# Optimization experiments

Measured on AMD Instinct MI355X. Metric: run time of the kernel, lower is better.

The kernel has to match this reference:

```python
import jax, jax.numpy as jnp
import numpy as np
from itertools import product

N = 300000          # active voxels
CIN, C = 16, 32     # input / conv channels
K = 27              # 3x3x3 kernel volume
Z, Y, X = 41, 1024, 1024  # sparse spatial shape (grid_size[::-1] + [1,0,0])
B = 2               # batch size
EPS = 1e-3          # BatchNorm eps (matches norm_fn eps=0.001)


def _build_coords_and_rulebook(rng):
    # unique active coords per batch element
    total = Z * Y * X
    per = N // B
    coords = []
    for b in range(B):
        lin = np.unique(rng.integers(0, total, size=int(per * 1.3)))
        rng.shuffle(lin)
        lin = lin[:per]
        assert lin.shape[0] == per
        z = lin // (Y * X)
        y = (lin % (Y * X)) // X
        x = lin % X
        coords.append(np.stack([np.full(per, b), z, y, x], axis=1))
    coords = np.concatenate(coords, axis=0).astype(np.int64)  # [N,4]

    # hash-free rulebook via sorted linear keys + searchsorted
    key = ((coords[:, 0] * Z + coords[:, 1]) * Y + coords[:, 2]) * X + coords[:, 3]
    perm = np.argsort(key)
    skey = key[perm]
    nbr = np.full((N, K), -1, dtype=np.int32)
    bz, zz, yy, xx = coords[:, 0], coords[:, 1], coords[:, 2], coords[:, 3]
    for k, (dz, dy, dx) in enumerate(product((-1, 0, 1), repeat=3)):
        nz, ny, nx = zz + dz, yy + dy, xx + dx
        valid = (nz >= 0) & (nz < Z) & (ny >= 0) & (ny < Y) & (nx >= 0) & (nx < X)
        nkey = ((bz * Z + nz) * Y + ny) * X + nx
        pos = np.searchsorted(skey, nkey)
        pos = np.clip(pos, 0, N - 1)
        found = valid & (skey[pos] == nkey)
        nbr[:, k] = np.where(found, perm[pos], -1).astype(np.int32)
    return coords, nbr


def _bn_params(k, c):
    k1, k2, k3, k4 = jax.random.split(k, 4)
    gamma = jax.random.uniform(k1, (c,), minval=0.5, maxval=1.5)
    beta = jax.random.normal(k2, (c,)) * 0.1
    mean = jax.random.normal(k3, (c,)) * 0.1
    var = jax.random.uniform(k4, (c,), minval=0.5, maxval=1.5)
    return jnp.stack([gamma, beta, mean, var], axis=0)  # [4,C]


def setup_inputs() -> dict:
    rng = np.random.default_rng(0)
    _, nbr = _build_coords_and_rulebook(rng)

    key = jax.random.key(0)
    ks = jax.random.split(key, 12)
    feat = jax.random.normal(ks[0], (N, CIN), dtype=jnp.float32)

    def conv_w(k, cin, cout):
        return jax.random.normal(k, (K, cin, cout), dtype=jnp.float32) * (1.0 / np.sqrt(K * cin))

    return {
        "voxel_features": feat,
        "neighbor_idx": jnp.asarray(nbr),
        "w_in": conv_w(ks[1], CIN, C), "bn_in": _bn_params(ks[2], C),
        "w1a": conv_w(ks[3], C, C), "bn1a": _bn_params(ks[4], C),
        "w1b": conv_w(ks[5], C, C), "bn1b": _bn_params(ks[6], C),
        "w2a": conv_w(ks[7], C, C), "bn2a": _bn_params(ks[8], C),
        "w2b": conv_w(ks[9], C, C), "bn2b": _bn_params(ks[10], C),
    }


def reference(voxel_features, neighbor_idx, w_in, bn_in, w1a, bn1a, w1b, bn1b,
              w2a, bn2a, w2b, bn2b):
    def bn(x, p):
        gamma, beta, mean, var = p
        return gamma * (x - mean) * jax.lax.rsqrt(var + EPS) + beta

    def subm(feat, w):
        # submanifold conv: gather active neighbors, GEMM per kernel offset, accumulate
        out = jnp.zeros((feat.shape[0], w.shape[2]), feat.dtype)
        for k in range(K):
            idx = neighbor_idx[:, k]
            g = jnp.where((idx >= 0)[:, None], feat[jnp.maximum(idx, 0)], 0.0)
            out = out + g @ w[k]
        return out

    # conv_input: SubMConv3d + BN + ReLU
    x = jax.nn.relu(bn(subm(voxel_features, w_in), bn_in))
    # conv1: two SparseBasicBlocks (conv-bn-relu-conv-bn + residual, relu)
    for wa, bna, wb, bnb in ((w1a, bn1a, w1b, bn1b), (w2a, bn2a, w2b, bn2b)):
        identity = x
        x = jax.nn.relu(bn(subm(x, wa), bna))
        x = bn(subm(x, wb), bnb)
        x = jax.nn.relu(x + identity)
    # voxel importance (vis_importance branch, minus file IO / sorting side effects)
    voxel_importance = jax.nn.sigmoid(jnp.mean(jnp.abs(x), axis=1, keepdims=True))
    return x, voxel_importance
```

## Files before the change

### kernel.cpp

```cpp
#include <hip/hip_runtime.h>
#include <hip/hip_bf16.h>
#include <hip/hip_fp16.h>
#include <cstdint>
#include <cstddef>

#define NVOX 300000
#define KNBR 27
#define COUT 32
#define CINP 32
#define NT   (NVOX / 16)
#define RB   ((NVOX + 255) / 256)
#define WFIXE (5 * KNBR * CINP * COUT)
#define WFB  ((WFIXE + 255) / 256)
#define WDE  (5 * COUT * CINP)
#define WDB  ((WDE + 255) / 256)
#define WPL  (KNBR * CINP * COUT)
#define GD   1172
#define GF0  876

typedef __hip_bfloat16 bf16;
typedef _Float16 half8 __attribute__((ext_vector_type(8)));
typedef float floatx4 __attribute__((ext_vector_type(4)));
typedef unsigned short ushort8 __attribute__((ext_vector_type(8)));

__device__ __forceinline__ float bf2f(unsigned short u) {
    union { unsigned int i; float f; } x; x.i = ((unsigned int)u) << 16; return x.f;
}
__device__ __forceinline__ int detect_fp32(const void* b0) {
    const unsigned short* p = (const unsigned short*)b0;
    int hits = 0;
    for (int i = 0; i < 16; i++) {
        float v = bf2f(p[2 * i]);
        if (v >= 0.25f && v <= 4.0f) hits++;
    }
    return (hits >= 8) ? 0 : 1;
}
__device__ __forceinline__ float rdw(const void* w, int rel, int fp32) {
    return fp32 ? ((const float*)w)[rel] : __bfloat162float(((const bf16*)w)[rel]);
}


__global__ __launch_bounds__(256)
void setup_kernel(const int* __restrict__ nbr,
                  const void* w0, const void* w1, const void* w2, const void* w3, const void* w4,
                  const void* b0, const void* b1, const void* b2, const void* b3, const void* b4,
                  float* __restrict__ wfix, __half* __restrict__ wtf,
                  float* __restrict__ bnab,
                  int* __restrict__ flag, int* __restrict__ counter,
                  int* __restrict__ cvlist, int* __restrict__ corrpos) {
    const int tid = threadIdx.x;

    if (blockIdx.x < RB) {
        __shared__ int flags[256];
        __shared__ int wsum[4];
        __shared__ int wbase[4];
        flags[tid] = 0;
        __syncthreads();
        const int base = blockIdx.x * 256;
        const int nvox = (NVOX - base < 256) ? (NVOX - base) : 256;
        const int nI4  = (nvox * KNBR) >> 2;
        const int4* p4 = (const int4*)(nbr + (size_t)base * KNBR);
        for (int i = tid; i < nI4; i += 256) {
            const int4 q = p4[i];
            if ((q.x & q.y & q.z & q.w) < 0) continue;
            const unsigned t = (unsigned)(i << 2);
            if (q.x >= 0) { unsigned u = t;     unsigned lv = (u * 4855u) >> 17; if (u - lv * 27u != 13u) flags[lv] = 1; }
            if (q.y >= 0) { unsigned u = t + 1; unsigned lv = (u * 4855u) >> 17; if (u - lv * 27u != 13u) flags[lv] = 1; }
            if (q.z >= 0) { unsigned u = t + 2; unsigned lv = (u * 4855u) >> 17; if (u - lv * 27u != 13u) flags[lv] = 1; }
            if (q.w >= 0) { unsigned u = t + 3; unsigned lv = (u * 4855u) >> 17; if (u - lv * 27u != 13u) flags[lv] = 1; }
        }
        __syncthreads();
        const int v = base + tid;
        const bool f = (tid < nvox) && (flags[tid] != 0);
        const unsigned long long wm = __ballot(f);
        const int wd = tid >> 6, ln = tid & 63;
        if (ln == 0) wsum[wd] = __popcll(wm);
        __syncthreads();
        if (tid == 0) {
            int t0 = wsum[0], t1 = wsum[1], t2 = wsum[2], t3 = wsum[3];
            int tot = t0 + t1 + t2 + t3;
            int b = tot ? atomicAdd(counter, tot) : 0;
            wbase[0] = b; wbase[1] = b + t0; wbase[2] = b + t0 + t1; wbase[3] = b + t0 + t1 + t2;
        }
        __syncthreads();
        if (f) {
            int pos = wbase[wd] + __popcll(wm & ((1ULL << ln) - 1ULL));
            cvlist[pos] = v;
            corrpos[v]  = pos;
        }
        return;
    }

    const int fp32 = detect_fp32(b0);

    if (blockIdx.x < RB + WFB) {
        int i = (blockIdx.x - RB) * 256 + tid;
        if (i >= WFIXE) return;
        int L   = i / (KNBR * CINP * COUT);
        int rem = i % (KNBR * CINP * COUT);
        int k   = rem / (CINP * COUT);
        int kk  = (rem / COUT) % CINP;
        int nn  = rem % COUT;
        const void* w = (L == 0) ? w0 : (L == 1) ? w1 : (L == 2) ? w2 : (L == 3) ? w3 : w4;
        int cinL = (L == 0) ? 16 : 32;
        wfix[i] = (kk < cinL) ? rdw(w, (k * cinL + kk) * COUT + nn, fp32) : 0.f;
        return;
    }

    if (blockIdx.x < RB + WFB + WDB) {
        int i = (blockIdx.x - RB - WFB) * 256 + tid;
        if (i >= WDE) return;
        int L  = i / (COUT * CINP);
        int nn = (i / CINP) % COUT;
        int kk = i % CINP;
        const void* w = (L == 0) ? w0 : (L == 1) ? w1 : (L == 2) ? w2 : (L == 3) ? w3 : w4;
        int cinL = (L == 0) ? 16 : 32;
        int sk = (L == 0) ? kk : ((kk & 1) ? 16 + (kk >> 1) : (kk >> 1));
        float val = (sk < cinL) ? rdw(w, (13 * cinL + sk) * COUT + nn, fp32) : 0.f;
        wtf[i] = __float2half(val);
        return;
    }

    if (tid == 192) *flag = fp32;
    if (tid < 160) {
        int L = tid / 32, c = tid % 32;
        const void* b = (L == 0) ? b0 : (L == 1) ? b1 : (L == 2) ? b2 : (L == 3) ? b3 : b4;
        float g, be, m, v;
        if (fp32) {
            const float* q = (const float*)b;
            g = q[c]; be = q[32 + c]; m = q[64 + c]; v = q[96 + c];
        } else {
            const bf16* q = (const bf16*)b;
            g = __bfloat162float(q[c]); be = __bfloat162float(q[32 + c]);
            m = __bfloat162float(q[64 + c]); v = __bfloat162float(q[96 + c]);
        }
        float a = g * rsqrtf(v + 1e-3f);
        bnab[L * 64 + c]      = a;
        bnab[L * 64 + 32 + c] = be - a * m;
    }
}


struct DW {
    half8 wa[5], wb[5];
    float ba[5], bb[5], bc[5], bd[5];
};
__device__ __forceinline__ void load_dw(DW& d, const __half* __restrict__ wtf,
                                        const float* __restrict__ bnab, int n, int quad) {
#pragma unroll
    for (int L = 0; L < 5; L++) {
        d.wa[L] = *(const half8*)((const _Float16*)wtf + L * 1024 + n * 32 + quad * 8);
        d.wb[L] = *(const half8*)((const _Float16*)wtf + L * 1024 + (n + 16) * 32 + quad * 8);
        d.ba[L] = bnab[L * 64 + n];      d.bb[L] = bnab[L * 64 + 32 + n];
        d.bc[L] = bnab[L * 64 + 16 + n]; d.bd[L] = bnab[L * 64 + 48 + n];
    }
}

__device__ __forceinline__ void dense_range(
    int gw, int nw, const DW& dw,
    const void* __restrict__ feat, int fp32, void* __restrict__ out_base,
    _Float16 (* __restrict__ myT)[40], int n, int quad) {
    for (int t = gw; t < NT; t += nw) {
        const int v0 = t * 16;
        half8 af = {};
        if (quad < 2) {
            if (fp32) {
                const float* p = (const float*)feat + (size_t)(v0 + n) * 16 + quad * 8;
                const float4 u0 = *(const float4*)p;
                const float4 u1 = *(const float4*)(p + 4);
                af[0] = (_Float16)u0.x; af[1] = (_Float16)u0.y; af[2] = (_Float16)u0.z; af[3] = (_Float16)u0.w;
                af[4] = (_Float16)u1.x; af[5] = (_Float16)u1.y; af[6] = (_Float16)u1.z; af[7] = (_Float16)u1.w;
            } else {
                const ushort8 u = *(const ushort8*)((const unsigned short*)feat + (size_t)(v0 + n) * 16 + quad * 8);
#pragma unroll
                for (int j = 0; j < 8; j++) af[j] = (_Float16)bf2f(u[j]);
            }
        }
        float id0[4], id1[4];
#pragma unroll
        for (int L = 0; L < 5; L++) {
            floatx4 c0 = {0.f, 0.f, 0.f, 0.f}, c1 = {0.f, 0.f, 0.f, 0.f};
            c0 = __builtin_amdgcn_mfma_f32_16x16x32_f16(af, dw.wa[L], c0, 0, 0, 0);
            c1 = __builtin_amdgcn_mfma_f32_16x16x32_f16(af, dw.wb[L], c1, 0, 0, 0);
            if (L < 4) {
#pragma unroll
                for (int r = 0; r < 4; r++) {
                    float y0 = fmaf(dw.ba[L], c0[r], dw.bb[L]);
                    float y1 = fmaf(dw.bc[L], c1[r], dw.bd[L]);
                    if (L == 2) { y0 += id0[r]; y1 += id1[r]; }
                    y0 = fmaxf(y0, 0.f); y1 = fmaxf(y1, 0.f);
                    if (L == 0 || L == 2) { id0[r] = y0; id1[r] = y1; }
                    const int m = quad * 4 + r;
                    *reinterpret_cast<__half2*>(&myT[m][2 * n]) = __floats2half2_rn(y0, y1);
                }
                af = *reinterpret_cast<const half8*>(&myT[n][quad * 8]);
            } else {
#pragma unroll
                for (int r = 0; r < 4; r++) {
                    float y0 = fmaxf(fmaf(dw.ba[4], c0[r], dw.bb[4]) + id0[r], 0.f);
                    float y1 = fmaxf(fmaf(dw.bc[4], c1[r], dw.bd[4]) + id1[r], 0.f);
                    const int v = v0 + quad * 4 + r;
                    float s = y0 + y1;
#pragma unroll
                    for (int o = 1; o < 16; o <<= 1) s += __shfl_xor(s, o, 16);
                    const float imp = 1.0f / (1.0f + expf(-s * (1.0f / 32.0f)));
                    if (fp32) {
                        float* ox = (float*)out_base;
                        ox[(size_t)v * COUT + n]      = y0;
                        ox[(size_t)v * COUT + n + 16] = y1;
                        if (n == 0) ox[(size_t)NVOX * COUT + v] = imp;
                    } else {
                        bf16* ox = (bf16*)out_base;
                        ox[(size_t)v * COUT + n]      = __float2bfloat16(y0);
                        ox[(size_t)v * COUT + n + 16] = __float2bfloat16(y1);
                        if (n == 0) ox[(size_t)NVOX * COUT + v] = __float2bfloat16(imp);
                    }
                }
            }
        }
    }
}

__device__ __forceinline__ void fix0_range(
    int nC, int gw, int nw, int lane,
    const void* __restrict__ feat, const int* __restrict__ nbr,
    const int* __restrict__ cvlist, const int* __restrict__ corrpos,
    int* __restrict__ ctap,
    const float* __restrict__ wt, const float* __restrict__ bnab,
    __half* __restrict__ xout, int fp32) {
    const int c = lane & 31;
    for (int i = gw; i < nC; i += nw) {
        const int v = cvlist[i];
        int idx = (lane < KNBR) ? nbr[(size_t)v * KNBR + lane] : -1;
        const bool valid = idx >= 0;
        unsigned long long m = __ballot(valid) & ((1ULL << KNBR) - 1ULL);
        if (valid) {
            int sp  = corrpos[idx];
            int pos = __popcll(m & ((1ULL << lane) - 1ULL));
            ctap[(size_t)i * 28 + 1 + pos] = (sp << 5) | lane;
        }
        if (lane == 0) ctap[(size_t)i * 28] = __popcll(m);
        float acc0 = 0.f, acc1 = 0.f;
        while (m) {
            const int k0 = (int)__builtin_ctzll(m); m &= m - 1;
            int k1 = -1;
            if (m) { k1 = (int)__builtin_ctzll(m); m &= m - 1; }
            const int kme = (lane >= 32) ? k1 : k0;
            const bool act = (kme >= 0);
            const int kk = act ? kme : 0;
            const int src = __shfl(idx, kk, 64);
            float xv = 0.f;
            if (act && c < 16)
                xv = fp32 ? ((const float*)feat)[(size_t)src * 16 + c]
                          : bf2f(((const unsigned short*)feat)[(size_t)src * 16 + c]);
            const float* wk = wt + (size_t)kk * (CINP * COUT) + c;
#pragma unroll
            for (int j = 0; j < 16; j += 2) {
                float xa = __shfl(xv, j, 32);
                float xb = __shfl(xv, j + 1, 32);
                acc0 = fmaf(xa, wk[j * COUT], acc0);
                acc1 = fmaf(xb, wk[(j + 1) * COUT], acc1);
            }
        }
        float acc = acc0 + acc1;
        acc += __shfl_xor(acc, 32, 64);
        float y = fmaxf(fmaf(bnab[c], acc, bnab[32 + c]), 0.f);
        if (lane < 32) xout[(size_t)i * COUT + c] = __float2half(y);
    }
}

template<int HAS_RES, int FINAL>
__device__ __forceinline__ void fixc_range(
    int nC, int gw, int nw, int lane,
    const __half* __restrict__ xin, const int* __restrict__ ctap,
    const int* __restrict__ cvlist,
    const float* __restrict__ wt, const float* __restrict__ bnab,
    const __half* __restrict__ res,
    __half* __restrict__ xout, void* __restrict__ out_base, int fp32io) {
    const int c = lane & 31;
    for (int i = gw; i < nC; i += nw) {
        const size_t tb = (size_t)i * 28;
        const int cnt = ctap[tb];
        const int tp  = (lane < cnt) ? ctap[tb + 1 + lane] : 0;
        float acc0 = 0.f, acc1 = 0.f;
        for (int t = 0; t < cnt; t += 2) {
            const bool actB = (t + 1) < cnt;
            const int sel = (lane >= 32 && actB) ? (t + 1) : t;
            const int tap = __shfl(tp, sel, 64);
            const bool act = (lane < 32) || actB;
            const int sp = tap >> 5, kk = tap & 31;
            const float xv = act ? __half2float(xin[(size_t)sp * COUT + c]) : 0.f;
            const float* wk = wt + (size_t)kk * (CINP * COUT) + c;
#pragma unroll
            for (int j = 0; j < 32; j += 2) {
                float xa = __shfl(xv, j, 32);
                float xb = __shfl(xv, j + 1, 32);
                acc0 = fmaf(xa, wk[j * COUT], acc0);
                acc1 = fmaf(xb, wk[(j + 1) * COUT], acc1);
            }
        }
        float acc = acc0 + acc1;
        acc += __shfl_xor(acc, 32, 64);
        float y = fmaf(bnab[c], acc, bnab[32 + c]);
        if (HAS_RES) y += __half2float(res[(size_t)i * COUT + c]);
        y = fmaxf(y, 0.f);

        if (FINAL) {
            float s2 = y;
#pragma unroll
            for (int o = 16; o > 0; o >>= 1) s2 += __shfl_xor(s2, o, 32);
            float imp = 1.0f / (1.0f + expf(-s2 * (1.0f / 32.0f)));
            const int v = cvlist[i];
            if (fp32io) {
                float* ox = (float*)out_base;
                if (lane < 32) ox[(size_t)v * COUT + c] = y;
                if (lane == 0) ox[(size_t)NVOX * COUT + v] = imp;
            } else {
                bf16* ox = (bf16*)out_base;
                if (lane < 32) ox[(size_t)v * COUT + c] = __float2bfloat16(y);
                if (lane == 0) ox[(size_t)NVOX * COUT + v] = __float2bfloat16(imp);
            }
        } else {
            if (lane < 32) xout[(size_t)i * COUT + c] = __float2half(y);
        }
    }
}


__global__ __launch_bounds__(256)
void phase0_kernel(const void* __restrict__ feat, const int* __restrict__ nbr,
                   const int* __restrict__ cvlist, const int* __restrict__ corrpos,
                   const int* __restrict__ counter, int* __restrict__ ctap,
                   const float* __restrict__ wfix, const __half* __restrict__ wtf,
                   const float* __restrict__ bnab,
                   __half* __restrict__ Xc0, void* __restrict__ out_base,
                   const int* __restrict__ flag) {
    __shared__ __align__(16) _Float16 ldsT[4][16][40];
    const int lane = threadIdx.x & 63;
    const int fp32 = *flag;
    if (blockIdx.x < GD) {
        const int gw = (blockIdx.x * 256 + threadIdx.x) >> 6;
        const int nw = (GD * 256) >> 6;
        const int wv = threadIdx.x >> 6;
        const int n = lane & 15, quad = lane >> 4;
        DW dw; load_dw(dw, wtf, bnab, n, quad);
        dense_range(gw, nw, dw, feat, fp32, out_base, ldsT[wv], n, quad);
    } else {
        const int gw = ((blockIdx.x - GD) * 256 + threadIdx.x) >> 6;
        const int nw = (GF0 * 256) >> 6;
        fix0_range(*counter, gw, nw, lane, feat, nbr, cvlist, corrpos, ctap,
                   wfix, bnab, Xc0, fp32);
    }
}

template<int HAS_RES, int FINAL>
__global__ __launch_bounds__(256)
void fixc_kernel(const __half* __restrict__ xin, const int* __restrict__ ctap,
                 const int* __restrict__ cvlist, const int* __restrict__ count,
                 const float* __restrict__ wt, const float* __restrict__ bnab,
                 const __half* __restrict__ res, __half* __restrict__ xout,
                 void* __restrict__ out_base, const int* __restrict__ flag) {
    const int gw   = (blockIdx.x * 256 + threadIdx.x) >> 6;
    const int nw   = (gridDim.x * 256) >> 6;
    const int lane = threadIdx.x & 63;
    fixc_range<HAS_RES, FINAL>(*count, gw, nw, lane, xin, ctap, cvlist, wt, bnab,
                               res, xout, out_base, *flag);
}

extern "C" void kernel_launch(void* const* d_in, const int* in_sizes, int n_in,
                              void* d_out, int out_size, void* d_ws, size_t ws_size,
                              hipStream_t stream) {
    char* ws = (char*)d_ws;
    int*    counter = (int*)ws;
    int*    flag    = counter + 1;
    int*    cvlist  = (int*)(ws + 256);
    int*    corrpos = cvlist + NVOX;
    int*    ctap    = corrpos + NVOX;
    float*  wfix    = (float*)(ctap + (size_t)NVOX * 28);
    float*  bnab    = wfix + WFIXE;
    __half* wtf     = (__half*)(bnab + 320);
    char*   after   = (char*)(wtf + WDE);
    __half* Xc0 = (__half*)((((uintptr_t)after) + 255) & ~(uintptr_t)255);
    __half* Xc1 = Xc0 + (size_t)NVOX * COUT;
    __half* Xc2 = Xc1 + (size_t)NVOX * COUT;

    const void* feat = d_in[0];
    const int*  nbr  = (const int*)d_in[1];

    hipMemsetAsync(counter, 0, 8, stream);

    setup_kernel<<<dim3(RB + WFB + WDB + 1), 256, 0, stream>>>(
        nbr, d_in[2], d_in[4], d_in[6], d_in[8], d_in[10],
        d_in[3], d_in[5], d_in[7], d_in[9], d_in[11],
        wfix, wtf, bnab, flag, counter, cvlist, corrpos);

    phase0_kernel<<<dim3(GD + GF0), 256, 0, stream>>>(
        feat, nbr, cvlist, corrpos, counter, ctap, wfix, wtf, bnab, Xc0, d_out, flag);

    dim3 gf(2048);
    fixc_kernel<0, 0><<<gf, 256, 0, stream>>>(Xc0, ctap, cvlist, counter, wfix + 1 * WPL, bnab + 1 * 64, nullptr, Xc1, nullptr, flag);
    fixc_kernel<1, 0><<<gf, 256, 0, stream>>>(Xc1, ctap, cvlist, counter, wfix + 2 * WPL, bnab + 2 * 64, Xc0,     Xc2, nullptr, flag);
    fixc_kernel<0, 0><<<gf, 256, 0, stream>>>(Xc2, ctap, cvlist, counter, wfix + 3 * WPL, bnab + 3 * 64, nullptr, Xc1, nullptr, flag);
    fixc_kernel<1, 1><<<gf, 256, 0, stream>>>(Xc1, ctap, cvlist, counter, wfix + 4 * WPL, bnab + 4 * 64, Xc2, nullptr, d_out, flag);
}
```

Before: 221.9 us.

## Fuse each basic block's two sparse convs into one kernel with recomputation

Replaces the four per-conv kernels with two kernels, each computing a whole SparseBasicBlock. For every output voxel and tap, the intermediate activation of the first conv is recomputed on the fly and immediately consumed by the second conv. This removes two launches and one intermediate buffer round-trip, but redoes the first conv's work once per neighbor tap (roughly the average neighbor count), which adds a lot of gather and FMA work. It also hoists the BN scale and shift loads out of the per-voxel loop in the first-layer path.

New measurement: 247.4 us. +11.5%, slower.

```diff
diff --git a/kernel.cpp b/kernel.cpp
--- a/kernel.cpp
+++ b/kernel.cpp
@@ -229,6 +229,7 @@
     const float* __restrict__ wt, const float* __restrict__ bnab,
     __half* __restrict__ xout, int fp32) {
     const int c = lane & 31;
+    const float bna = bnab[c], bnb = bnab[32 + c];
     for (int i = gw; i < nC; i += nw) {
         const int v = cvlist[i];
         int idx = (lane < KNBR) ? nbr[(size_t)v * KNBR + lane] : -1;
@@ -264,65 +265,8 @@
         }
         float acc = acc0 + acc1;
         acc += __shfl_xor(acc, 32, 64);
-        float y = fmaxf(fmaf(bnab[c], acc, bnab[32 + c]), 0.f);
+        float y = fmaxf(fmaf(bna, acc, bnb), 0.f);
         if (lane < 32) xout[(size_t)i * COUT + c] = __float2half(y);
-    }
-}
-
-template<int HAS_RES, int FINAL>
-__device__ __forceinline__ void fixc_range(
-    int nC, int gw, int nw, int lane,
-    const __half* __restrict__ xin, const int* __restrict__ ctap,
-    const int* __restrict__ cvlist,
-    const float* __restrict__ wt, const float* __restrict__ bnab,
-    const __half* __restrict__ res,
-    __half* __restrict__ xout, void* __restrict__ out_base, int fp32io) {
-    const int c = lane & 31;
-    for (int i = gw; i < nC; i += nw) {
-        const size_t tb = (size_t)i * 28;
-        const int cnt = ctap[tb];
-        const int tp  = (lane < cnt) ? ctap[tb + 1 + lane] : 0;
-        float acc0 = 0.f, acc1 = 0.f;
-        for (int t = 0; t < cnt; t += 2) {
-            const bool actB = (t + 1) < cnt;
-            const int sel = (lane >= 32 && actB) ? (t + 1) : t;
-            const int tap = __shfl(tp, sel, 64);
-            const bool act = (lane < 32) || actB;
-            const int sp = tap >> 5, kk = tap & 31;
-            const float xv = act ? __half2float(xin[(size_t)sp * COUT + c]) : 0.f;
-            const float* wk = wt + (size_t)kk * (CINP * COUT) + c;
-#pragma unroll
-            for (int j = 0; j < 32; j += 2) {
-                float xa = __shfl(xv, j, 32);
-                float xb = __shfl(xv, j + 1, 32);
-                acc0 = fmaf(xa, wk[j * COUT], acc0);
-                acc1 = fmaf(xb, wk[(j + 1) * COUT], acc1);
-            }
-        }
-        float acc = acc0 + acc1;
-        acc += __shfl_xor(acc, 32, 64);
-        float y = fmaf(bnab[c], acc, bnab[32 + c]);
-        if (HAS_RES) y += __half2float(res[(size_t)i * COUT + c]);
-        y = fmaxf(y, 0.f);
-
-        if (FINAL) {
-            float s2 = y;
-#pragma unroll
-            for (int o = 16; o > 0; o >>= 1) s2 += __shfl_xor(s2, o, 32);
-            float imp = 1.0f / (1.0f + expf(-s2 * (1.0f / 32.0f)));
-            const int v = cvlist[i];
-            if (fp32io) {
-                float* ox = (float*)out_base;
-                if (lane < 32) ox[(size_t)v * COUT + c] = y;
-                if (lane == 0) ox[(size_t)NVOX * COUT + v] = imp;
-            } else {
-                bf16* ox = (bf16*)out_base;
-                if (lane < 32) ox[(size_t)v * COUT + c] = __float2bfloat16(y);
-                if (lane == 0) ox[(size_t)NVOX * COUT + v] = __float2bfloat16(imp);
-            }
-        } else {
-            if (lane < 32) xout[(size_t)i * COUT + c] = __float2half(y);
-        }
     }
 }
 
@@ -353,18 +297,86 @@
     }
 }
 
-template<int HAS_RES, int FINAL>
+template<int FINAL>
 __global__ __launch_bounds__(256)
-void fixc_kernel(const __half* __restrict__ xin, const int* __restrict__ ctap,
-                 const int* __restrict__ cvlist, const int* __restrict__ count,
-                 const float* __restrict__ wt, const float* __restrict__ bnab,
-                 const __half* __restrict__ res, __half* __restrict__ xout,
-                 void* __restrict__ out_base, const int* __restrict__ flag) {
+void fixpair_kernel(const __half* __restrict__ xin, const int* __restrict__ ctap,
+                    const int* __restrict__ cvlist, const int* __restrict__ count,
+                    const float* __restrict__ wA, const float* __restrict__ bnA,
+                    const float* __restrict__ wB, const float* __restrict__ bnB,
+                    __half* __restrict__ xout, void* __restrict__ out_base,
+                    const int* __restrict__ flag) {
     const int gw   = (blockIdx.x * 256 + threadIdx.x) >> 6;
     const int nw   = (gridDim.x * 256) >> 6;
     const int lane = threadIdx.x & 63;
-    fixc_range<HAS_RES, FINAL>(*count, gw, nw, lane, xin, ctap, cvlist, wt, bnab,
-                               res, xout, out_base, *flag);
+    const int c    = lane & 31;
+    const int hf   = lane >> 5;
+    const int nC   = *count;
+    const int fp32io = FINAL ? *flag : 0;
+    const float bnAa = bnA[c], bnAb = bnA[32 + c];
+    const float bnBa = bnB[c], bnBb = bnB[32 + c];
+    const int j0 = hf * 16;
+
+    for (int i = gw; i < nC; i += nw) {
+        const size_t tbi = (size_t)i * 28;
+        const int cnt = ctap[tbi];
+        const int tpi = (lane < cnt) ? ctap[tbi + 1 + lane] : 0;
+        float acc0 = 0.f, acc1 = 0.f;
+        for (int t = 0; t < cnt; ++t) {
+            const int tap = __shfl(tpi, t, 64);
+            const int sp = tap >> 5, kt = tap & 31;
+            const size_t tbs = (size_t)sp * 28;
+            const int cs = ctap[tbs];
+            const int tps = (lane < cs) ? ctap[tbs + 1 + lane] : 0;
+            float ia0 = 0.f, ia1 = 0.f;
+            for (int u = 0; u < cs; u += 2) {
+                const bool b2 = (u + 1) < cs;
+                const int tapu = __shfl(tps, (hf && b2) ? u + 1 : u, 64);
+                const bool act = (hf == 0) || b2;
+                const int spu = tapu >> 5, ku = tapu & 31;
+                const float xv = act ? __half2float(xin[(size_t)spu * COUT + c]) : 0.f;
+                const float* wk = wA + (size_t)ku * (CINP * COUT) + c;
+#pragma unroll
+                for (int j = 0; j < 32; j += 2) {
+                    ia0 = fmaf(__shfl(xv, j, 32),     wk[j * COUT],       ia0);
+                    ia1 = fmaf(__shfl(xv, j + 1, 32), wk[(j + 1) * COUT], ia1);
+                }
+            }
+            float ia = ia0 + ia1;
+            ia += __shfl_xor(ia, 32, 64);
+            const float z = fmaxf(fmaf(bnAa, ia, bnAb), 0.f);
+            const float* wkb = wB + (size_t)kt * (CINP * COUT) + c;
+#pragma unroll
+            for (int jj = 0; jj < 16; jj += 2) {
+                const int j = j0 + jj;
+                acc0 = fmaf(__shfl(z, j, 32),     wkb[j * COUT],       acc0);
+                acc1 = fmaf(__shfl(z, j + 1, 32), wkb[(j + 1) * COUT], acc1);
+            }
+        }
+        float acc = acc0 + acc1;
+        acc += __shfl_xor(acc, 32, 64);
+        float y = fmaf(bnBa, acc, bnBb);
+        y += __half2float(xin[(size_t)i * COUT + c]);
+        y = fmaxf(y, 0.f);
+
+        if (FINAL) {
+            float s2 = y;
+#pragma unroll
+            for (int o = 16; o > 0; o >>= 1) s2 += __shfl_xor(s2, o, 32);
+            const float imp = 1.0f / (1.0f + expf(-s2 * (1.0f / 32.0f)));
+            const int v = cvlist[i];
+            if (fp32io) {
+                float* ox = (float*)out_base;
+                if (lane < 32) ox[(size_t)v * COUT + c] = y;
+                if (lane == 0) ox[(size_t)NVOX * COUT + v] = imp;
+            } else {
+                bf16* ox = (bf16*)out_base;
+                if (lane < 32) ox[(size_t)v * COUT + c] = __float2bfloat16(y);
+                if (lane == 0) ox[(size_t)NVOX * COUT + v] = __float2bfloat16(imp);
+            }
+        } else {
+            if (lane < 32) xout[(size_t)i * COUT + c] = __float2half(y);
+        }
+    }
 }
 
 extern "C" void kernel_launch(void* const* d_in, const int* in_sizes, int n_in,
@@ -381,8 +393,7 @@
     __half* wtf     = (__half*)(bnab + 320);
     char*   after   = (char*)(wtf + WDE);
     __half* Xc0 = (__half*)((((uintptr_t)after) + 255) & ~(uintptr_t)255);
-    __half* Xc1 = Xc0 + (size_t)NVOX * COUT;
-    __half* Xc2 = Xc1 + (size_t)NVOX * COUT;
+    __half* Xc2 = Xc0 + (size_t)NVOX * COUT;
 
     const void* feat = d_in[0];
     const int*  nbr  = (const int*)d_in[1];
@@ -398,8 +409,8 @@
         feat, nbr, cvlist, corrpos, counter, ctap, wfix, wtf, bnab, Xc0, d_out, flag);
 
     dim3 gf(2048);
-    fixc_kernel<0, 0><<<gf, 256, 0, stream>>>(Xc0, ctap, cvlist, counter, wfix + 1 * WPL, bnab + 1 * 64, nullptr, Xc1, nullptr, flag);
-    fixc_kernel<1, 0><<<gf, 256, 0, stream>>>(Xc1, ctap, cvlist, counter, wfix + 2 * WPL, bnab + 2 * 64, Xc0,     Xc2, nullptr, flag);
-    fixc_kernel<0, 0><<<gf, 256, 0, stream>>>(Xc2, ctap, cvlist, counter, wfix + 3 * WPL, bnab + 3 * 64, nullptr, Xc1, nullptr, flag);
-    fixc_kernel<1, 1><<<gf, 256, 0, stream>>>(Xc1, ctap, cvlist, counter, wfix + 4 * WPL, bnab + 4 * 64, Xc2, nullptr, d_out, flag);
-}
+    fixpair_kernel<0><<<gf, 256, 0, stream>>>(Xc0, ctap, cvlist, counter,
+        wfix + 1 * WPL, bnab + 1 * 64, wfix + 2 * WPL, bnab + 2 * 64, Xc2, nullptr, flag);
+    fixpair_kernel<1><<<gf, 256, 0, stream>>>(Xc2, ctap, cvlist, counter,
+        wfix + 3 * WPL, bnab + 3 * 64, wfix + 4 * WPL, bnab + 4 * 64, nullptr, d_out, flag);
+}
```

## Collapse isolated voxel pairs into a fused five-layer closed-form pass

Applied to the files above, without the earlier changes.

Setup now counts each voxel's non-center neighbors. Voxels whose only neighbor is a single mutual partner form isolated pairs; these are taken out of the per-layer conv kernels and computed in one final kernel that runs all five layers for both members in registers. The remaining complex voxels go into a compacted list processed by the middle layers, which cuts their gather work and their intermediate reads and writes. Grid splits were retuned as well. The cost is atomic list building, extra workspace, and divergent work mixed inside the final kernel.

Result: slower. 359.2 us (+61.8%).

```diff
diff --git a/kernel.cpp b/kernel.cpp
--- a/kernel.cpp
+++ b/kernel.cpp
@@ -15,8 +15,8 @@
 #define WDE  (5 * COUT * CINP)
 #define WDB  ((WDE + 255) / 256)
 #define WPL  (KNBR * CINP * COUT)
-#define GD   1172
-#define GF0  876
+#define GD   1536
+#define GF0  512
 
 typedef __hip_bfloat16 bf16;
 typedef _Float16 half8 __attribute__((ext_vector_type(8)));
@@ -47,7 +47,8 @@
                   float* __restrict__ wfix, __half* __restrict__ wtf,
                   float* __restrict__ bnab,
                   int* __restrict__ flag, int* __restrict__ counter,
-                  int* __restrict__ cvlist, int* __restrict__ corrpos) {
+                  int* __restrict__ cvlist, int* __restrict__ corrpos,
+                  unsigned char* __restrict__ nnarr) {
     const int tid = threadIdx.x;
 
     if (blockIdx.x < RB) {
@@ -64,14 +65,17 @@
             const int4 q = p4[i];
             if ((q.x & q.y & q.z & q.w) < 0) continue;
             const unsigned t = (unsigned)(i << 2);
-            if (q.x >= 0) { unsigned u = t;     unsigned lv = (u * 4855u) >> 17; if (u - lv * 27u != 13u) flags[lv] = 1; }
-            if (q.y >= 0) { unsigned u = t + 1; unsigned lv = (u * 4855u) >> 17; if (u - lv * 27u != 13u) flags[lv] = 1; }
-            if (q.z >= 0) { unsigned u = t + 2; unsigned lv = (u * 4855u) >> 17; if (u - lv * 27u != 13u) flags[lv] = 1; }
-            if (q.w >= 0) { unsigned u = t + 3; unsigned lv = (u * 4855u) >> 17; if (u - lv * 27u != 13u) flags[lv] = 1; }
+            if (q.x >= 0) { unsigned u = t;     unsigned lv = (u * 4855u) >> 17; if (u - lv * 27u != 13u) atomicAdd(&flags[lv], 1); }
+            if (q.y >= 0) { unsigned u = t + 1; unsigned lv = (u * 4855u) >> 17; if (u - lv * 27u != 13u) atomicAdd(&flags[lv], 1); }
+            if (q.z >= 0) { unsigned u = t + 2; unsigned lv = (u * 4855u) >> 17; if (u - lv * 27u != 13u) atomicAdd(&flags[lv], 1); }
+            if (q.w >= 0) { unsigned u = t + 3; unsigned lv = (u * 4855u) >> 17; if (u - lv * 27u != 13u) atomicAdd(&flags[lv], 1); }
         }
         __syncthreads();
         const int v = base + tid;
-        const bool f = (tid < nvox) && (flags[tid] != 0);
+        const int nn = flags[tid];
+        const bool inr = (tid < nvox);
+        if (inr) nnarr[v] = (unsigned char)(nn > 255 ? 255 : nn);
+        const bool f = inr && (nn > 0);
         const unsigned long long wm = __ballot(f);
         const int wd = tid >> 6, ln = tid & 63;
         if (ln == 0) wsum[wd] = __popcll(wm);
@@ -225,15 +229,33 @@
     int nC, int gw, int nw, int lane,
     const void* __restrict__ feat, const int* __restrict__ nbr,
     const int* __restrict__ cvlist, const int* __restrict__ corrpos,
-    int* __restrict__ ctap,
+    const unsigned char* __restrict__ nnarr,
+    int* __restrict__ ctap, int* __restrict__ clist, int* __restrict__ ccount,
+    int* __restrict__ plist, int* __restrict__ pcount,
     const float* __restrict__ wt, const float* __restrict__ bnab,
     __half* __restrict__ xout, int fp32) {
     const int c = lane & 31;
+    const float bna = bnab[c], bnb = bnab[32 + c];
     for (int i = gw; i < nC; i += nw) {
         const int v = cvlist[i];
         int idx = (lane < KNBR) ? nbr[(size_t)v * KNBR + lane] : -1;
         const bool valid = idx >= 0;
         unsigned long long m = __ballot(valid) & ((1ULL << KNBR) - 1ULL);
+        const unsigned long long mnb = m & ~(1ULL << 13);
+        const int nn = __popcll(mnb);
+        if (nn == 1) {
+            const int k = (int)__builtin_ctzll(mnb);
+            const int u = __shfl(idx, k, 64);
+            if (nnarr[u] == 1) {
+                if (lane == 0 && v < u) {
+                    int p = atomicAdd(pcount, 1);
+                    plist[2 * p]     = (v << 5) | k;
+                    plist[2 * p + 1] = u;
+                }
+                continue;
+            }
+        }
+        if (lane == 0) { int p = atomicAdd(ccount, 1); clist[p] = i; }
         if (valid) {
             int sp  = corrpos[idx];
             int pos = __popcll(m & ((1ULL << lane) - 1ULL));
@@ -264,65 +286,8 @@
         }
         float acc = acc0 + acc1;
         acc += __shfl_xor(acc, 32, 64);
-        float y = fmaxf(fmaf(bnab[c], acc, bnab[32 + c]), 0.f);
+        float y = fmaxf(fmaf(bna, acc, bnb), 0.f);
         if (lane < 32) xout[(size_t)i * COUT + c] = __float2half(y);
-    }
-}
-
-template<int HAS_RES, int FINAL>
-__device__ __forceinline__ void fixc_range(
-    int nC, int gw, int nw, int lane,
-    const __half* __restrict__ xin, const int* __restrict__ ctap,
-    const int* __restrict__ cvlist,
-    const float* __restrict__ wt, const float* __restrict__ bnab,
-    const __half* __restrict__ res,
-    __half* __restrict__ xout, void* __restrict__ out_base, int fp32io) {
-    const int c = lane & 31;
-    for (int i = gw; i < nC; i += nw) {
-        const size_t tb = (size_t)i * 28;
-        const int cnt = ctap[tb];
-        const int tp  = (lane < cnt) ? ctap[tb + 1 + lane] : 0;
-        float acc0 = 0.f, acc1 = 0.f;
-        for (int t = 0; t < cnt; t += 2) {
-            const bool actB = (t + 1) < cnt;
-            const int sel = (lane >= 32 && actB) ? (t + 1) : t;
-            const int tap = __shfl(tp, sel, 64);
-            const bool act = (lane < 32) || actB;
-            const int sp = tap >> 5, kk = tap & 31;
-            const float xv = act ? __half2float(xin[(size_t)sp * COUT + c]) : 0.f;
-            const float* wk = wt + (size_t)kk * (CINP * COUT) + c;
-#pragma unroll
-            for (int j = 0; j < 32; j += 2) {
-                float xa = __shfl(xv, j, 32);
-                float xb = __shfl(xv, j + 1, 32);
-                acc0 = fmaf(xa, wk[j * COUT], acc0);
-                acc1 = fmaf(xb, wk[(j + 1) * COUT], acc1);
-            }
-        }
-        float acc = acc0 + acc1;
-        acc += __shfl_xor(acc, 32, 64);
-        float y = fmaf(bnab[c], acc, bnab[32 + c]);
-        if (HAS_RES) y += __half2float(res[(size_t)i * COUT + c]);
-        y = fmaxf(y, 0.f);
-
-        if (FINAL) {
-            float s2 = y;
-#pragma unroll
-            for (int o = 16; o > 0; o >>= 1) s2 += __shfl_xor(s2, o, 32);
-            float imp = 1.0f / (1.0f + expf(-s2 * (1.0f / 32.0f)));
-            const int v = cvlist[i];
-            if (fp32io) {
-                float* ox = (float*)out_base;
-                if (lane < 32) ox[(size_t)v * COUT + c] = y;
-                if (lane == 0) ox[(size_t)NVOX * COUT + v] = imp;
-            } else {
-                bf16* ox = (bf16*)out_base;
-                if (lane < 32) ox[(size_t)v * COUT + c] = __float2bfloat16(y);
-                if (lane == 0) ox[(size_t)NVOX * COUT + v] = __float2bfloat16(imp);
-            }
-        } else {
-            if (lane < 32) xout[(size_t)i * COUT + c] = __float2half(y);
-        }
     }
 }
 
@@ -330,7 +295,10 @@
 __global__ __launch_bounds__(256)
 void phase0_kernel(const void* __restrict__ feat, const int* __restrict__ nbr,
                    const int* __restrict__ cvlist, const int* __restrict__ corrpos,
+                   const unsigned char* __restrict__ nnarr,
                    const int* __restrict__ counter, int* __restrict__ ctap,
+                   int* __restrict__ clist, int* __restrict__ ccount,
+                   int* __restrict__ plist, int* __restrict__ pcount,
                    const float* __restrict__ wfix, const __half* __restrict__ wtf,
                    const float* __restrict__ bnab,
                    __half* __restrict__ Xc0, void* __restrict__ out_base,
@@ -348,23 +316,159 @@
     } else {
         const int gw = ((blockIdx.x - GD) * 256 + threadIdx.x) >> 6;
         const int nw = (GF0 * 256) >> 6;
-        fix0_range(*counter, gw, nw, lane, feat, nbr, cvlist, corrpos, ctap,
-                   wfix, bnab, Xc0, fp32);
-    }
-}
-
-template<int HAS_RES, int FINAL>
+        fix0_range(*counter, gw, nw, lane, feat, nbr, cvlist, corrpos, nnarr,
+                   ctap, clist, ccount, plist, pcount, wfix, bnab, Xc0, fp32);
+    }
+}
+
+template<int HAS_RES>
 __global__ __launch_bounds__(256)
-void fixc_kernel(const __half* __restrict__ xin, const int* __restrict__ ctap,
-                 const int* __restrict__ cvlist, const int* __restrict__ count,
+void fixs_kernel(const __half* __restrict__ xin, const int* __restrict__ ctap,
+                 const int* __restrict__ clist, const int* __restrict__ ccount,
                  const float* __restrict__ wt, const float* __restrict__ bnab,
-                 const __half* __restrict__ res, __half* __restrict__ xout,
-                 void* __restrict__ out_base, const int* __restrict__ flag) {
+                 const __half* __restrict__ res, __half* __restrict__ xout) {
     const int gw   = (blockIdx.x * 256 + threadIdx.x) >> 6;
     const int nw   = (gridDim.x * 256) >> 6;
     const int lane = threadIdx.x & 63;
-    fixc_range<HAS_RES, FINAL>(*count, gw, nw, lane, xin, ctap, cvlist, wt, bnab,
-                               res, xout, out_base, *flag);
+    const int c    = lane & 31;
+    const int nC   = *ccount;
+    const float bna = bnab[c], bnb = bnab[32 + c];
+    for (int jj = gw; jj < nC; jj += nw) {
+        const int i = clist[jj];
+        const size_t tb = (size_t)i * 28;
+        const int cnt = ctap[tb];
+        const int tp  = ctap[tb + 1 + lane];
+        float acc0 = 0.f, acc1 = 0.f;
+        for (int t = 0; t < cnt; t += 2) {
+            const bool actB = (t + 1) < cnt;
+            const int sel = (lane >= 32 && actB) ? (t + 1) : t;
+            const int tap = __shfl(tp, sel, 64);
+            const bool act = (lane < 32) || actB;
+            const int sp = tap >> 5, kk = tap & 31;
+            const float xv = act ? __half2float(xin[(size_t)sp * COUT + c]) : 0.f;
+            const float* wk = wt + (size_t)kk * (CINP * COUT) + c;
+#pragma unroll
+            for (int j = 0; j < 32; j += 2) {
+                acc0 = fmaf(__shfl(xv, j, 32),     wk[j * COUT],       acc0);
+                acc1 = fmaf(__shfl(xv, j + 1, 32), wk[(j + 1) * COUT], acc1);
+            }
+        }
+        float acc = acc0 + acc1;
+        acc += __shfl_xor(acc, 32, 64);
+        float y = fmaf(bna, acc, bnb);
+        if (HAS_RES) y += __half2float(res[(size_t)i * COUT + c]);
+        y = fmaxf(y, 0.f);
+        if (lane < 32) xout[(size_t)i * COUT + c] = __float2half(y);
+    }
+}
+
+__global__ __launch_bounds__(256)
+void final_kernel(const void* __restrict__ feat,
+                  const int* __restrict__ plist, const int* __restrict__ pcount,
+                  const int* __restrict__ clist, const int* __restrict__ ccount,
+                  const int* __restrict__ ctap, const int* __restrict__ cvlist,
+                  const __half* __restrict__ Xc1, const __half* __restrict__ Xc2,
+                  const float* __restrict__ wfix, const float* __restrict__ bnab,
+                  void* __restrict__ out_base, const int* __restrict__ flag) {
+    const int gw   = (blockIdx.x * 256 + threadIdx.x) >> 6;
+    const int nw   = (gridDim.x * 256) >> 6;
+    const int lane = threadIdx.x & 63;
+    const int c    = lane & 31;
+    const int hf   = lane >> 5;
+    const int npair = *pcount, ncplx = *ccount;
+    const int total = npair + ncplx;
+    const int fp32io = *flag;
+
+    for (int j = gw; j < total; j += nw) {
+        if (j < npair) {
+            const int e0 = plist[2 * j], u = plist[2 * j + 1];
+            const int v = e0 >> 5, kv = e0 & 31;
+            const int myv = hf ? u : v;
+            const int myk = hf ? 26 - kv : kv;
+            float x = 0.f;
+            if (c < 16)
+                x = fp32io ? ((const float*)feat)[(size_t)myv * 16 + c]
+                           : bf2f(((const unsigned short*)feat)[(size_t)myv * 16 + c]);
+            float id = 0.f;
+#pragma unroll
+            for (int L = 0; L < 5; L++) {
+                const float* ws_ = wfix + L * WPL + 13 * (CINP * COUT) + c;
+                const float* wc_ = wfix + L * WPL + myk * (CINP * COUT) + c;
+                const int JL = (L == 0) ? 16 : 32;
+                float a0 = 0.f, a1 = 0.f;
+#pragma unroll
+                for (int jj = 0; jj < 32; jj += 2) {
+                    if (jj >= JL) break;
+                    const float s0 = __shfl(x, jj + hf * 32, 64);
+                    const float o0 = __shfl(x, jj + 32 - hf * 32, 64);
+                    a0 = fmaf(s0, ws_[jj * COUT], a0);
+                    a0 = fmaf(o0, wc_[jj * COUT], a0);
+                    const float s1 = __shfl(x, jj + 1 + hf * 32, 64);
+                    const float o1 = __shfl(x, jj + 1 + 32 - hf * 32, 64);
+                    a1 = fmaf(s1, ws_[(jj + 1) * COUT], a1);
+                    a1 = fmaf(o1, wc_[(jj + 1) * COUT], a1);
+                }
+                float t = fmaf(bnab[L * 64 + c], a0 + a1, bnab[L * 64 + 32 + c]);
+                if (L == 2 || L == 4) t += id;
+                t = fmaxf(t, 0.f);
+                if (L == 0 || L == 2) id = t;
+                x = t;
+            }
+            float s2 = x;
+#pragma unroll
+            for (int o = 16; o > 0; o >>= 1) s2 += __shfl_xor(s2, o, 32);
+            const float imp = 1.0f / (1.0f + expf(-s2 * (1.0f / 32.0f)));
+            if (fp32io) {
+                float* ox = (float*)out_base;
+                ox[(size_t)myv * COUT + c] = x;
+                if (c == 0) ox[(size_t)NVOX * COUT + myv] = imp;
+            } else {
+                bf16* ox = (bf16*)out_base;
+                ox[(size_t)myv * COUT + c] = __float2bfloat16(x);
+                if (c == 0) ox[(size_t)NVOX * COUT + myv] = __float2bfloat16(imp);
+            }
+        } else {
+            const int i = clist[j - npair];
+            const size_t tb = (size_t)i * 28;
+            const int cnt = ctap[tb];
+            const int tp  = ctap[tb + 1 + lane];
+            const float* wt = wfix + 4 * WPL;
+            float acc0 = 0.f, acc1 = 0.f;
+            for (int t = 0; t < cnt; t += 2) {
+                const bool actB = (t + 1) < cnt;
+                const int sel = (lane >= 32 && actB) ? (t + 1) : t;
+                const int tap = __shfl(tp, sel, 64);
+                const bool act = (lane < 32) || actB;
+                const int sp = tap >> 5, kk = tap & 31;
+                const float xv = act ? __half2float(Xc1[(size_t)sp * COUT + c]) : 0.f;
+                const float* wk = wt + (size_t)kk * (CINP * COUT) + c;
+#pragma unroll
+                for (int jq = 0; jq < 32; jq += 2) {
+                    acc0 = fmaf(__shfl(xv, jq, 32),     wk[jq * COUT],       acc0);
+                    acc1 = fmaf(__shfl(xv, jq + 1, 32), wk[(jq + 1) * COUT], acc1);
+                }
+            }
+            float acc = acc0 + acc1;
+            acc += __shfl_xor(acc, 32, 64);
+            float y = fmaf(bnab[4 * 64 + c], acc, bnab[4 * 64 + 32 + c]);
+            y += __half2float(Xc2[(size_t)i * COUT + c]);
+            y = fmaxf(y, 0.f);
+            float s2 = y;
+#pragma unroll
+            for (int o = 16; o > 0; o >>= 1) s2 += __shfl_xor(s2, o, 32);
+            const float imp = 1.0f / (1.0f + expf(-s2 * (1.0f / 32.0f)));
+            const int v = cvlist[i];
+            if (fp32io) {
+                float* ox = (float*)out_base;
+                if (lane < 32) ox[(size_t)v * COUT + c] = y;
+                if (lane == 0) ox[(size_t)NVOX * COUT + v] = imp;
+            } else {
+                bf16* ox = (bf16*)out_base;
+                if (lane < 32) ox[(size_t)v * COUT + c] = __float2bfloat16(y);
+                if (lane == 0) ox[(size_t)NVOX * COUT + v] = __float2bfloat16(imp);
+            }
+        }
+    }
 }
 
 extern "C" void kernel_launch(void* const* d_in, const int* in_sizes, int n_in,
@@ -373,33 +477,43 @@
     char* ws = (char*)d_ws;
     int*    counter = (int*)ws;
     int*    flag    = counter + 1;
+    int*    pcount  = counter + 2;
+    int*    ccount  = counter + 3;
     int*    cvlist  = (int*)(ws + 256);
     int*    corrpos = cvlist + NVOX;
-    int*    ctap    = corrpos + NVOX;
-    float*  wfix    = (float*)(ctap + (size_t)NVOX * 28);
+    int*    clist   = corrpos + NVOX;
+    int*    plist   = clist + NVOX;
+    unsigned char* nnarr = (unsigned char*)(plist + NVOX);
+    uintptr_t pa    = (((uintptr_t)(nnarr + NVOX)) + 255) & ~(uintptr_t)255;
+    int*    ctap    = (int*)pa;
+    float*  wfix    = (float*)(ctap + (size_t)NVOX * 28 + 64);
     float*  bnab    = wfix + WFIXE;
     __half* wtf     = (__half*)(bnab + 320);
-    char*   after   = (char*)(wtf + WDE);
-    __half* Xc0 = (__half*)((((uintptr_t)after) + 255) & ~(uintptr_t)255);
+    uintptr_t xa    = (((uintptr_t)(wtf + WDE)) + 255) & ~(uintptr_t)255;
+    __half* Xc0 = (__half*)xa;
     __half* Xc1 = Xc0 + (size_t)NVOX * COUT;
     __half* Xc2 = Xc1 + (size_t)NVOX * COUT;
 
     const void* feat = d_in[0];
     const int*  nbr  = (const int*)d_in[1];
 
-    hipMemsetAsync(counter, 0, 8, stream);
+    hipMemsetAsync(counter, 0, 16, stream);
 
     setup_kernel<<<dim3(RB + WFB + WDB + 1), 256, 0, stream>>>(
         nbr, d_in[2], d_in[4], d_in[6], d_in[8], d_in[10],
         d_in[3], d_in[5], d_in[7], d_in[9], d_in[11],
-        wfix, wtf, bnab, flag, counter, cvlist, corrpos);
+        wfix, wtf, bnab, flag, counter, cvlist, corrpos, nnarr);
 
     phase0_kernel<<<dim3(GD + GF0), 256, 0, stream>>>(
-        feat, nbr, cvlist, corrpos, counter, ctap, wfix, wtf, bnab, Xc0, d_out, flag);
-
-    dim3 gf(2048);
-    fixc_kernel<0, 0><<<gf, 256, 0, stream>>>(Xc0, ctap, cvlist, counter, wfix + 1 * WPL, bnab + 1 * 64, nullptr, Xc1, nullptr, flag);
-    fixc_kernel<1, 0><<<gf, 256, 0, stream>>>(Xc1, ctap, cvlist, counter, wfix + 2 * WPL, bnab + 2 * 64, Xc0,     Xc2, nullptr, flag);
-    fixc_kernel<0, 0><<<gf, 256, 0, stream>>>(Xc2, ctap, cvlist, counter, wfix + 3 * WPL, bnab + 3 * 64, nullptr, Xc1, nullptr, flag);
-    fixc_kernel<1, 1><<<gf, 256, 0, stream>>>(Xc1, ctap, cvlist, counter, wfix + 4 * WPL, bnab + 4 * 64, Xc2, nullptr, d_out, flag);
-}
+        feat, nbr, cvlist, corrpos, nnarr, counter, ctap, clist, ccount,
+        plist, pcount, wfix, wtf, bnab, Xc0, d_out, flag);
+
+    dim3 gs(1024);
+    fixs_kernel<0><<<gs, 256, 0, stream>>>(Xc0, ctap, clist, ccount, wfix + 1 * WPL, bnab + 1 * 64, nullptr, Xc1);
+    fixs_kernel<1><<<gs, 256, 0, stream>>>(Xc1, ctap, clist, ccount, wfix + 2 * WPL, bnab + 2 * 64, Xc0,     Xc2);
+    fixs_kernel<0><<<gs, 256, 0, stream>>>(Xc2, ctap, clist, ccount, wfix + 3 * WPL, bnab + 3 * 64, nullptr, Xc1);
+
+    final_kernel<<<dim3(2048), 256, 0, stream>>>(
+        feat, plist, pcount, clist, ccount, ctap, cvlist, Xc1, Xc2,
+        wfix, bnab, d_out, flag);
+}
```
